# Optimization experiments

Hardware: AMD Instinct MI355X
Metric: run time of the kernel (lower is better)

Reference implementation:

```python
import jax, jax.numpy as jnp
import numpy as np

N, D, K = 32768, 512, 8192
TOPK = 3
BETA = 0.25  # commitment_cost
EPS = 1e-12  # F.normalize eps


def setup_inputs() -> dict:
    key = jax.random.key(0)
    k1, k2 = jax.random.split(key)
    x = jax.random.normal(k1, (N, D), dtype=jnp.float32)
    # nn.Embedding weight init: uniform(-1/num_embeddings, 1/num_embeddings)
    embeddings = jax.random.uniform(k2, (K, D), dtype=jnp.float32,
                                    minval=-1.0 / K, maxval=1.0 / K)
    return {"x": x, "embeddings": embeddings}


def _l2_normalize(v, axis):
    n = jnp.sqrt(jnp.sum(v * v, axis=axis, keepdims=True))
    return v / jnp.maximum(n, EPS)


def reference(x, embeddings):
    # --- get_code_indices ---
    xn = _l2_normalize(x, axis=1)              # [N, D]
    wn = _l2_normalize(embeddings, axis=1)     # [K, D]
    # squared euclidean distance between normalized vectors
    distances = (jnp.sum(xn * xn, axis=1, keepdims=True)
                 + jnp.sum(wn * wn, axis=1)
                 - 2.0 * jnp.einsum('nd,kd->nk', xn, wn))   # [N, K]
    neg_top, top_indices = jax.lax.top_k(-distances, TOPK)   # smallest distances
    top_values = -neg_top                                    # [N, TOPK]
    inv = 1.0 / top_values
    weights = inv / jnp.sum(inv, axis=1, keepdims=True)      # [N, TOPK]
    # --- quantize: gather UN-normalized codebook rows, weighted sum ---
    topk_quantized = embeddings[top_indices]                 # [N, TOPK, D]
    quantized = jnp.sum(topk_quantized * weights[..., None], axis=1)  # [N, D]
    # --- training losses + straight-through estimator ---
    q_latent_loss = jnp.mean((quantized - jax.lax.stop_gradient(x)) ** 2)
    e_latent_loss = jnp.mean((x - jax.lax.stop_gradient(quantized)) ** 2)
    loss = q_latent_loss + BETA * e_latent_loss
    quantized_st = x + jax.lax.stop_gradient(quantized - x)
    return quantized_st, loss, top_indices
```

## Files before the change

kernel.cpp:

```cpp
#include <hip/hip_runtime.h>
#include <cstdint>
#include <cstddef>

#define N_ROWS  32768
#define DIMS    512
#define K_CODES 8192

typedef short    bf16x8 __attribute__((ext_vector_type(8)));
typedef float    f32x4  __attribute__((ext_vector_type(4)));

__device__ __forceinline__ unsigned short cvt_bf16_rne(float f) {
  union { float f; unsigned u; } c; c.f = f;
  unsigned r = c.u + 0x7FFFu + ((c.u >> 16) & 1u);
  return (unsigned short)(r >> 16);
}


__device__ __forceinline__ float np_pairwise_sumsq_512(const float* buf, int l) {
  int blk = l >> 4, jv = (l >> 2) & 3, ln = l & 3;
  int cb = blk * 128 + jv * 4 + ln;
  float v = buf[cb];
  float r = __fmul_rn(v, v);
  #pragma unroll
  for (int i = 1; i < 8; ++i) {
    float t = buf[cb + 16 * i];
    r = __fadd_rn(r, __fmul_rn(t, t));
  }
  r = __fadd_rn(r, __shfl_xor(r, 4, 64));
  r = __fadd_rn(r, __shfl_xor(r, 8, 64));
  r = __fadd_rn(r, __shfl_xor(r, 1, 64));
  r = __fadd_rn(r, __shfl_xor(r, 2, 64));
  r = __fadd_rn(r, __shfl_xor(r, 16, 64));
  r = __fadd_rn(r, __shfl_xor(r, 32, 64));
  return r;
}

__global__ __launch_bounds__(256) void prep_x_kernel(
    const float* __restrict__ x, float* __restrict__ xninv) {
  int row = blockIdx.x * 4 + (threadIdx.x >> 6);
  int l = threadIdx.x & 63;
  const float* xr = x + (size_t)row * DIMS + l * 8;
  float4 a = *(const float4*)xr;
  float4 b = *(const float4*)(xr + 4);
  float s = a.x*a.x + a.y*a.y + a.z*a.z + a.w*a.w
          + b.x*b.x + b.y*b.y + b.z*b.z + b.w*b.w;
  #pragma unroll
  for (int off = 1; off < 64; off <<= 1) s += __shfl_xor(s, off, 64);
  float den = fmaxf(sqrtf(s), 1e-12f);
  if (l == 0) xninv[row] = 1.0f / den;
}

__global__ __launch_bounds__(256) void prep_w_np_kernel(
    const float* __restrict__ emb, float* __restrict__ den_w,
    float* __restrict__ wnorm2, unsigned short* __restrict__ wnh) {
  __shared__ float buf[4][512];
  int w = threadIdx.x >> 6, l = threadIdx.x & 63;
  int row = blockIdx.x * 4 + w;
  const float* wr = emb + (size_t)row * DIMS + l * 8;
  float4 a = *(const float4*)wr;
  float4 b = *(const float4*)(wr + 4);
  *(float4*)&buf[w][l * 8]     = a;
  *(float4*)&buf[w][l * 8 + 4] = b;
  __syncthreads();
  float S = np_pairwise_sumsq_512(buf[w], l);
  float den = fmaxf(__fsqrt_rn(S), 1e-12f);
  float nv[8];
  nv[0] = __fdiv_rn(a.x, den); nv[1] = __fdiv_rn(a.y, den);
  nv[2] = __fdiv_rn(a.z, den); nv[3] = __fdiv_rn(a.w, den);
  nv[4] = __fdiv_rn(b.x, den); nv[5] = __fdiv_rn(b.y, den);
  nv[6] = __fdiv_rn(b.z, den); nv[7] = __fdiv_rn(b.w, den);
  __syncthreads();
  *(float4*)&buf[w][l * 8]     = float4{nv[0], nv[1], nv[2], nv[3]};
  *(float4*)&buf[w][l * 8 + 4] = float4{nv[4], nv[5], nv[6], nv[7]};
  {
    unsigned hv[4];
    #pragma unroll
    for (int j = 0; j < 4; ++j) {
      unsigned lo = cvt_bf16_rne(nv[2*j]);
      unsigned hi = cvt_bf16_rne(nv[2*j + 1]);
      hv[j] = lo | (hi << 16);
    }
    *(uint4*)(wnh + (size_t)row * DIMS + l * 8) =
        uint4{hv[0], hv[1], hv[2], hv[3]};
  }
  __syncthreads();
  float S2 = np_pairwise_sumsq_512(buf[w], l);
  if (l == 0) { wnorm2[row] = S2; den_w[row] = den; }
}

#define MT_ROWS 128
#define MT_TILES 32
#define NSPLIT 4
#define SPLIT_COLS 2048
#define NROWGRP (N_ROWS / MT_ROWS)
#define BSTR_B 272
#define DSTR   33
#define QSTRIDE 32

__global__
__attribute__((amdgpu_flat_work_group_size(256, 256), amdgpu_waves_per_eu(2, 2)))
void mfma_topk_kernel(
    const float* __restrict__ x, const unsigned short* __restrict__ wnh,
    const float* __restrict__ xninv, unsigned* __restrict__ candk,
    unsigned* __restrict__ qctr) {
  __shared__ unsigned short Bs[64 * (BSTR_B / 2)];
  unsigned* dump = (unsigned*)Bs;
  __shared__ int s_rg, s_sp;

  const int tid = threadIdx.x;
  const int lane = tid & 63;
  const int wv = tid >> 6;
  const int l15 = lane & 15;
  const int lq = lane >> 4;

  if (tid == 0) {
    unsigned xcc;
    asm("s_getreg_b32 %0, hwreg(HW_REG_XCC_ID)" : "=s"(xcc));
    const int mysplit = (int)(xcc & 3);
    int rg = -1, sp = 0;
    #pragma unroll 1
    for (int i = 0; i < NSPLIT; ++i) {
      int s = (mysplit + i) & (NSPLIT - 1);
      unsigned r = atomicAdd(&qctr[s * QSTRIDE], 1u);
      if (r < (unsigned)NROWGRP) { rg = (int)r; sp = s; break; }
    }
    s_rg = rg; s_sp = sp;
  }
  __syncthreads();
  const int rowgrp = s_rg;
  const int split = s_sp;
  if (rowgrp < 0) return;
  const int row0 = rowgrp * MT_ROWS;
  const int col0 = split * SPLIT_COLS;

  const int scol = tid >> 2;
  const int spart = tid & 3;

  bf16x8 afrag[2][16];
  #pragma unroll
  for (int rs = 0; rs < 2; ++rs) {
    int row = row0 + wv * 32 + rs * 16 + l15;
    float sc = xninv[row];
    const float* xp = x + (size_t)row * DIMS + lq * 8;
    #pragma unroll
    for (int ks = 0; ks < 16; ++ks) {
      float4 a = *(const float4*)(xp + ks * 32);
      float4 b = *(const float4*)(xp + ks * 32 + 4);
      bf16x8 f;
      f[0] = (short)cvt_bf16_rne(a.x * sc); f[1] = (short)cvt_bf16_rne(a.y * sc);
      f[2] = (short)cvt_bf16_rne(a.z * sc); f[3] = (short)cvt_bf16_rne(a.w * sc);
      f[4] = (short)cvt_bf16_rne(b.x * sc); f[5] = (short)cvt_bf16_rne(b.y * sc);
      f[6] = (short)cvt_bf16_rne(b.z * sc); f[7] = (short)cvt_bf16_rne(b.w * sc);
      afrag[rs][ks] = f;
    }
  }

  unsigned m[8];
  #pragma unroll
  for (int j = 0; j < 8; ++j) m[j] = 0u;

  uint4 s0, s1, s2, s3;
  {
    const char* p = (const char*)wnh
        + ((size_t)(col0 + scol) * DIMS) * 2 + spart * 64;
    s0 = *(const uint4*)(p);
    s1 = *(const uint4*)(p + 16);
    s2 = *(const uint4*)(p + 32);
    s3 = *(const uint4*)(p + 48);
  }

  for (int t = 0; t < MT_TILES; ++t) {
    f32x4 acc[2][4];
    #pragma unroll
    for (int rs = 0; rs < 2; ++rs)
      #pragma unroll
      for (int cs = 0; cs < 4; ++cs)
        acc[rs][cs] = f32x4{0.f, 0.f, 0.f, 0.f};

    #pragma unroll
    for (int c = 0; c < 4; ++c) {
      __syncthreads();
      char* dst = (char*)Bs + scol * BSTR_B + spart * 64;
      *(uint4*)(dst)      = s0;
      *(uint4*)(dst + 16) = s1;
      *(uint4*)(dst + 32) = s2;
      *(uint4*)(dst + 48) = s3;
      int nt = t + ((c + 1) >> 2);
      int nc = (c + 1) & 3;
      if (nt < MT_TILES) {
        const char* p = (const char*)wnh
            + ((size_t)(col0 + nt * 64 + scol) * DIMS) * 2
            + nc * 256 + spart * 64;
        s0 = *(const uint4*)(p);
        s1 = *(const uint4*)(p + 16);
        s2 = *(const uint4*)(p + 32);
        s3 = *(const uint4*)(p + 48);
      }
      __syncthreads();
      #pragma unroll
      for (int kk = 0; kk < 4; ++kk) {
        const int ks = c * 4 + kk;
        bf16x8 bfr[4];
        #pragma unroll
        for (int cs = 0; cs < 4; ++cs)
          bfr[cs] = *(const bf16x8*)((const char*)Bs
                      + (cs * 16 + l15) * BSTR_B + kk * 64 + lq * 16);
        #pragma unroll
        for (int rs = 0; rs < 2; ++rs)
          #pragma unroll
          for (int cs = 0; cs < 4; ++cs)
            acc[rs][cs] = __builtin_amdgcn_mfma_f32_16x16x32_bf16(
                afrag[rs][ks], bfr[cs], acc[rs][cs], 0, 0, 0);
      }
    }
    __syncthreads();

    #pragma unroll
    for (int rs = 0; rs < 2; ++rs)
      #pragma unroll
      for (int rg2 = 0; rg2 < 4; ++rg2) {
        unsigned kkey[4];
        #pragma unroll
        for (int cs = 0; cs < 4; ++cs) {
          float v = acc[rs][cs][rg2];
          union { float f; unsigned u; } cu;
          cu.f = fmaf(v, 0.5f, 2.5f);
          kkey[cs] = ((cu.u << 9) & 0xFFFFF000u)
                   | (unsigned)(t * 64 + cs * 16 + l15);
        }
        unsigned h1 = max(kkey[0], kkey[1]), lo1 = min(kkey[0], kkey[1]);
        unsigned h2 = max(kkey[2], kkey[3]), lo2 = min(kkey[2], kkey[3]);
        unsigned m1 = max(h1, h2);
        unsigned m2 = max(min(h1, h2), max(lo1, lo2));
        int rowl = wv * 32 + rs * 16 + lq * 4 + rg2;
        dump[rowl * DSTR + l15 * 2 + 0] = m1;
        dump[rowl * DSTR + l15 * 2 + 1] = m2;
      }
    __syncthreads();

    {
      int srow = tid & 127;
      int qb = (tid >> 7) * 16;
      #pragma unroll
      for (int q = 0; q < 16; ++q) {
        unsigned cv = dump[srow * DSTR + qb + q];
        #pragma unroll
        for (int j = 0; j < 8; ++j) {
          unsigned hi = max(m[j], cv), lo = min(m[j], cv);
          m[j] = hi; cv = lo;
        }
      }
    }
  }

  __syncthreads();
  if (tid >= 128) {
    #pragma unroll
    for (int j = 0; j < 8; ++j) dump[(tid & 127) * DSTR + 16 + j] = m[j];
  }
  __syncthreads();
  if (tid < 128) {
    #pragma unroll
    for (int j = 0; j < 8; ++j) {
      unsigned cv = dump[tid * DSTR + 16 + j];
      #pragma unroll
      for (int jj = 0; jj < 8; ++jj) {
        unsigned hi = max(m[jj], cv), lo = min(m[jj], cv);
        m[jj] = hi; cv = lo;
      }
    }
    unsigned* o = candk + (size_t)(row0 + tid) * 32 + split * 8;
    #pragma unroll
    for (int j = 0; j < 8; ++j) o[j] = m[j];
  }
}

#define WSTR 516

__global__ __launch_bounds__(256, 3) void refine_mfma_kernel(
    const float* __restrict__ x, const float* __restrict__ emb,
    const float* __restrict__ den_w, const float* __restrict__ wnorm2,
    const unsigned* __restrict__ candk,
    float* __restrict__ out, double* __restrict__ lossparts) {
  __shared__ float xbuf[4][512];
  __shared__ float wbuf4[4][4 * WSTR];
  int w = threadIdx.x >> 6, l = threadIdx.x & 63;
  int row = blockIdx.x * 4 + w;

  const float* xr = x + (size_t)row * DIMS + l * 8;
  float4 x0 = *(const float4*)xr;
  float4 x1 = *(const float4*)(xr + 4);
  *(float4*)&xbuf[w][l * 8]     = x0;
  *(float4*)&xbuf[w][l * 8 + 4] = x1;
  __syncthreads();
  float Sx = np_pairwise_sumsq_512(xbuf[w], l);
  float denx = fmaxf(__fsqrt_rn(Sx), 1e-12f);
  float xn[8];
  xn[0] = __fdiv_rn(x0.x, denx); xn[1] = __fdiv_rn(x0.y, denx);
  xn[2] = __fdiv_rn(x0.z, denx); xn[3] = __fdiv_rn(x0.w, denx);
  xn[4] = __fdiv_rn(x1.x, denx); xn[5] = __fdiv_rn(x1.y, denx);
  xn[6] = __fdiv_rn(x1.z, denx); xn[7] = __fdiv_rn(x1.w, denx);
  __syncthreads();
  *(float4*)&xbuf[w][l * 8]     = float4{xn[0], xn[1], xn[2], xn[3]};
  *(float4*)&xbuf[w][l * 8 + 4] = float4{xn[4], xn[5], xn[6], xn[7]};
  __syncthreads();
  float xn2 = np_pairwise_sumsq_512(xbuf[w], l);

  unsigned val = 0u; int col = 0x7fffffff;
  if (l < 32) {
    unsigned key = candk[(size_t)row * 32 + l];
    val = key >> 12;
    col = (l >> 3) * SPLIT_COLS + (int)(key & 0xFFFu);
  }

  int k8[8];
  #pragma unroll
  for (int it = 0; it < 8; ++it) {
    unsigned mv = val; int mk = col;
    #pragma unroll
    for (int off = 1; off < 64; off <<= 1) {
      unsigned ov = (unsigned)__shfl_xor((int)mv, off, 64);
      int ok = __shfl_xor(mk, off, 64);
      bool take = (ov > mv) || (ov == mv && ok < mk);
      mv = take ? ov : mv; mk = take ? ok : mk;
    }
    k8[it] = mk;
    if (col == mk) val = 0u;
  }

  float4 ga[4], gb[4];
  #pragma unroll
  for (int c = 0; c < 4; ++c) {
    const float* wr = emb + (size_t)k8[c] * DIMS + l * 8;
    ga[c] = *(const float4*)wr;
    gb[c] = *(const float4*)(wr + 4);
  }

  float d8[8];
  #pragma unroll
  for (int g = 0; g < 2; ++g) {
    #pragma unroll
    for (int c = 0; c < 4; ++c) {
      float dk = den_w[k8[g * 4 + c]];
      *(float4*)&wbuf4[w][c * WSTR + l * 8] =
          float4{__fdiv_rn(ga[c].x, dk), __fdiv_rn(ga[c].y, dk),
                 __fdiv_rn(ga[c].z, dk), __fdiv_rn(ga[c].w, dk)};
      *(float4*)&wbuf4[w][c * WSTR + l * 8 + 4] =
          float4{__fdiv_rn(gb[c].x, dk), __fdiv_rn(gb[c].y, dk),
                 __fdiv_rn(gb[c].z, dk), __fdiv_rn(gb[c].w, dk)};
    }
    if (g == 0) {
      #pragma unroll
      for (int c = 0; c < 4; ++c) {
        const float* wr = emb + (size_t)k8[4 + c] * DIMS + l * 8;
        ga[c] = *(const float4*)wr;
        gb[c] = *(const float4*)(wr + 4);
      }
    }
    __syncthreads();

    {
      int j = l & 3;
      const float* xp = xbuf[w];
      const float* wp = &wbuf4[w][j * WSTR];
      float t = 0.f;
      #pragma unroll 8
      for (int d = 0; d < 512; ++d) t = fmaf(xp[d], wp[d], t);
      #pragma unroll
      for (int c = 0; c < 4; ++c) {
        float dot = __shfl(t, c, 64);
        float s = __fadd_rn(xn2, wnorm2[k8[g * 4 + c]]);
        d8[g * 4 + c] = __fadd_rn(s, -(2.0f * dot));
      }
    }
    __syncthreads();
  }

  {
    float bd[3]; int bk[3];
    #pragma unroll
    for (int s = 0; s < 3; ++s) {
      float mv = INFINITY; int mk = 0x7fffffff;
      #pragma unroll
      for (int it = 0; it < 8; ++it) {
        bool take = (d8[it] < mv) || (d8[it] == mv && k8[it] < mk);
        mv = take ? d8[it] : mv; mk = take ? k8[it] : mk;
      }
      bd[s] = mv; bk[s] = mk;
      #pragma unroll
      for (int it = 0; it < 8; ++it)
        if (k8[it] == mk) d8[it] = INFINITY;
    }

    double i0 = 1.0 / (double)bd[0], i1 = 1.0 / (double)bd[1],
           i2 = 1.0 / (double)bd[2];
    double tot = (i0 + i1) + i2;
    double w0q = i0 / tot, w1q = i1 / tot, w2q = i2 / tot;

    if (l == 0) {
      float* oi = out + (size_t)N_ROWS * DIMS + 1 + (size_t)row * 3;
      oi[0] = (float)bk[0]; oi[1] = (float)bk[1]; oi[2] = (float)bk[2];
    }

    const float* e0 = emb + (size_t)bk[0] * DIMS + l * 8;
    const float* e1 = emb + (size_t)bk[1] * DIMS + l * 8;
    const float* e2 = emb + (size_t)bk[2] * DIMS + l * 8;
    float4 ea0 = *(const float4*)e0, eb0 = *(const float4*)(e0 + 4);
    float4 ea1 = *(const float4*)e1, eb1 = *(const float4*)(e1 + 4);
    float4 ea2 = *(const float4*)e2, eb2 = *(const float4*)(e2 + 4);
    double xs[8];
    xs[0] = x0.x; xs[1] = x0.y; xs[2] = x0.z; xs[3] = x0.w;
    xs[4] = x1.x; xs[5] = x1.y; xs[6] = x1.z; xs[7] = x1.w;
    double q[8];
    q[0] = w0q*(double)ea0.x + w1q*(double)ea1.x + w2q*(double)ea2.x;
    q[1] = w0q*(double)ea0.y + w1q*(double)ea1.y + w2q*(double)ea2.y;
    q[2] = w0q*(double)ea0.z + w1q*(double)ea1.z + w2q*(double)ea2.z;
    q[3] = w0q*(double)ea0.w + w1q*(double)ea1.w + w2q*(double)ea2.w;
    q[4] = w0q*(double)eb0.x + w1q*(double)eb1.x + w2q*(double)eb2.x;
    q[5] = w0q*(double)eb0.y + w1q*(double)eb1.y + w2q*(double)eb2.y;
    q[6] = w0q*(double)eb0.z + w1q*(double)eb1.z + w2q*(double)eb2.z;
    q[7] = w0q*(double)eb0.w + w1q*(double)eb1.w + w2q*(double)eb2.w;

    double lp = 0.0;
    float o[8];
    #pragma unroll
    for (int jj = 0; jj < 8; ++jj) {
      double diff = q[jj] - xs[jj];
      o[jj] = (float)(xs[jj] + diff);
      lp += diff * diff;
    }
    float* orow = out + (size_t)row * DIMS + l * 8;
    *(float4*)orow       = float4{o[0], o[1], o[2], o[3]};
    *(float4*)(orow + 4) = float4{o[4], o[5], o[6], o[7]};

    #pragma unroll
    for (int off = 1; off < 64; off <<= 1) lp += __shfl_xor(lp, off, 64);
    if (l == 0) lossparts[row] = lp;
  }
}

__global__ __launch_bounds__(256) void loss_finalize_kernel(
    const double* __restrict__ lossparts, float* __restrict__ out) {
  __shared__ double sred[4];
  int tid = threadIdx.x;
  double s = 0.0;
  for (int i = tid; i < N_ROWS; i += 256) s += lossparts[i];
  #pragma unroll
  for (int off = 1; off < 64; off <<= 1) s += __shfl_xor(s, off, 64);
  if ((tid & 63) == 0) sred[tid >> 6] = s;
  __syncthreads();
  if (tid == 0) {
    double m = (((sred[0] + sred[1]) + sred[2]) + sred[3]) / 16777216.0;
    out[(size_t)N_ROWS * DIMS] = (float)(m + 0.25 * m);
  }
}

extern "C" void kernel_launch(void* const* d_in, const int* in_sizes, int n_in,
                              void* d_out, int out_size, void* d_ws, size_t ws_size,
                              hipStream_t stream) {
  (void)in_sizes; (void)n_in; (void)out_size; (void)ws_size;
  const float* x   = (const float*)d_in[0];
  const float* emb = (const float*)d_in[1];
  float* out = (float*)d_out;
  char* ws = (char*)d_ws;

  float*          wnorm2    = (float*)(ws);
  float*          den_w     = (float*)(ws + 32768);
  float*          xninv     = (float*)(ws + 65536);
  unsigned short* wnh       = (unsigned short*)(ws + 196608);
  unsigned*       candk     = (unsigned*)(ws + 8585216);
  double*         lossparts = (double*)(ws + 12779520);
  unsigned*       qctr      = (unsigned*)(ws + 13041664);

  prep_w_np_kernel<<<K_CODES / 4, 256, 0, stream>>>(emb, den_w, wnorm2, wnh);
  prep_x_kernel<<<N_ROWS / 4, 256, 0, stream>>>(x, xninv);
  hipMemsetAsync(qctr, 0, 512, stream);
  mfma_topk_kernel<<<NROWGRP * NSPLIT, 256, 0, stream>>>(
      x, wnh, xninv, candk, qctr);
  refine_mfma_kernel<<<N_ROWS / 4, 256, 0, stream>>>(
      x, emb, den_w, wnorm2, candk, out, lossparts);
  loss_finalize_kernel<<<1, 256, 0, stream>>>(lossparts, out);
}
```

Before: 746.4 us.

## Use 512-thread blocks with one 16-row strip per wave in top-k GEMM

Block size of the MFMA top-k kernel doubles from 256 to 512 threads. Each of the 8 waves now owns 16 rows instead of 32, which halves the A-fragment and accumulator registers per wave, and the occupancy hint rises from 2 to 4 waves per EU. B-tile staging is split across twice as many threads, and the final merge now folds three partial top-8 lists into the first group. Each wave does half as many MFMAs per B-fragment load from LDS, so LDS read traffic per MFMA doubles and the serial final merge gets longer.

```diff
diff --git a/kernel.cpp b/kernel.cpp
--- a/kernel.cpp
+++ b/kernel.cpp
@@ -98,7 +98,7 @@
 #define QSTRIDE 32
 
 __global__
-__attribute__((amdgpu_flat_work_group_size(256, 256), amdgpu_waves_per_eu(2, 2)))
+__attribute__((amdgpu_flat_work_group_size(512, 512), amdgpu_waves_per_eu(4, 4)))
 void mfma_topk_kernel(
     const float* __restrict__ x, const unsigned short* __restrict__ wnh,
     const float* __restrict__ xninv, unsigned* __restrict__ candk,
@@ -133,13 +133,12 @@
   const int row0 = rowgrp * MT_ROWS;
   const int col0 = split * SPLIT_COLS;
 
-  const int scol = tid >> 2;
-  const int spart = tid & 3;
-
-  bf16x8 afrag[2][16];
-  #pragma unroll
-  for (int rs = 0; rs < 2; ++rs) {
-    int row = row0 + wv * 32 + rs * 16 + l15;
+  const int scol = tid >> 3;
+  const int spart = tid & 7;
+
+  bf16x8 afrag[16];
+  {
+    int row = row0 + wv * 16 + l15;
     float sc = xninv[row];
     const float* xp = x + (size_t)row * DIMS + lq * 8;
     #pragma unroll
@@ -151,7 +150,7 @@
       f[2] = (short)cvt_bf16_rne(a.z * sc); f[3] = (short)cvt_bf16_rne(a.w * sc);
       f[4] = (short)cvt_bf16_rne(b.x * sc); f[5] = (short)cvt_bf16_rne(b.y * sc);
       f[6] = (short)cvt_bf16_rne(b.z * sc); f[7] = (short)cvt_bf16_rne(b.w * sc);
-      afrag[rs][ks] = f;
+      afrag[ks] = f;
     }
   }
 
@@ -159,42 +158,34 @@
   #pragma unroll
   for (int j = 0; j < 8; ++j) m[j] = 0u;
 
-  uint4 s0, s1, s2, s3;
+  uint4 s0, s1;
   {
     const char* p = (const char*)wnh
-        + ((size_t)(col0 + scol) * DIMS) * 2 + spart * 64;
+        + ((size_t)(col0 + scol) * DIMS) * 2 + spart * 32;
     s0 = *(const uint4*)(p);
     s1 = *(const uint4*)(p + 16);
-    s2 = *(const uint4*)(p + 32);
-    s3 = *(const uint4*)(p + 48);
   }
 
   for (int t = 0; t < MT_TILES; ++t) {
-    f32x4 acc[2][4];
-    #pragma unroll
-    for (int rs = 0; rs < 2; ++rs)
-      #pragma unroll
-      for (int cs = 0; cs < 4; ++cs)
-        acc[rs][cs] = f32x4{0.f, 0.f, 0.f, 0.f};
+    f32x4 acc[4];
+    #pragma unroll
+    for (int cs = 0; cs < 4; ++cs)
+      acc[cs] = f32x4{0.f, 0.f, 0.f, 0.f};
 
     #pragma unroll
     for (int c = 0; c < 4; ++c) {
       __syncthreads();
-      char* dst = (char*)Bs + scol * BSTR_B + spart * 64;
+      char* dst = (char*)Bs + scol * BSTR_B + spart * 32;
       *(uint4*)(dst)      = s0;
       *(uint4*)(dst + 16) = s1;
-      *(uint4*)(dst + 32) = s2;
-      *(uint4*)(dst + 48) = s3;
       int nt = t + ((c + 1) >> 2);
       int nc = (c + 1) & 3;
       if (nt < MT_TILES) {
         const char* p = (const char*)wnh
             + ((size_t)(col0 + nt * 64 + scol) * DIMS) * 2
-            + nc * 256 + spart * 64;
+            + nc * 256 + spart * 32;
         s0 = *(const uint4*)(p);
         s1 = *(const uint4*)(p + 16);
-        s2 = *(const uint4*)(p + 32);
-        s3 = *(const uint4*)(p + 48);
       }
       __syncthreads();
       #pragma unroll
@@ -206,43 +197,39 @@
           bfr[cs] = *(const bf16x8*)((const char*)Bs
                       + (cs * 16 + l15) * BSTR_B + kk * 64 + lq * 16);
         #pragma unroll
-        for (int rs = 0; rs < 2; ++rs)
-          #pragma unroll
-          for (int cs = 0; cs < 4; ++cs)
-            acc[rs][cs] = __builtin_amdgcn_mfma_f32_16x16x32_bf16(
-                afrag[rs][ks], bfr[cs], acc[rs][cs], 0, 0, 0);
+        for (int cs = 0; cs < 4; ++cs)
+          acc[cs] = __builtin_amdgcn_mfma_f32_16x16x32_bf16(
+              afrag[ks], bfr[cs], acc[cs], 0, 0, 0);
       }
     }
     __syncthreads();
 
     #pragma unroll
-    for (int rs = 0; rs < 2; ++rs)
-      #pragma unroll
-      for (int rg2 = 0; rg2 < 4; ++rg2) {
-        unsigned kkey[4];
-        #pragma unroll
-        for (int cs = 0; cs < 4; ++cs) {
-          float v = acc[rs][cs][rg2];
-          union { float f; unsigned u; } cu;
-          cu.f = fmaf(v, 0.5f, 2.5f);
-          kkey[cs] = ((cu.u << 9) & 0xFFFFF000u)
-                   | (unsigned)(t * 64 + cs * 16 + l15);
-        }
-        unsigned h1 = max(kkey[0], kkey[1]), lo1 = min(kkey[0], kkey[1]);
-        unsigned h2 = max(kkey[2], kkey[3]), lo2 = min(kkey[2], kkey[3]);
-        unsigned m1 = max(h1, h2);
-        unsigned m2 = max(min(h1, h2), max(lo1, lo2));
-        int rowl = wv * 32 + rs * 16 + lq * 4 + rg2;
-        dump[rowl * DSTR + l15 * 2 + 0] = m1;
-        dump[rowl * DSTR + l15 * 2 + 1] = m2;
-      }
+    for (int rg2 = 0; rg2 < 4; ++rg2) {
+      unsigned kkey[4];
+      #pragma unroll
+      for (int cs = 0; cs < 4; ++cs) {
+        float v = acc[cs][rg2];
+        union { float f; unsigned u; } cu;
+        cu.f = fmaf(v, 0.5f, 2.5f);
+        kkey[cs] = ((cu.u << 9) & 0xFFFFF000u)
+                 | (unsigned)(t * 64 + cs * 16 + l15);
+      }
+      unsigned h1 = max(kkey[0], kkey[1]), lo1 = min(kkey[0], kkey[1]);
+      unsigned h2 = max(kkey[2], kkey[3]), lo2 = min(kkey[2], kkey[3]);
+      unsigned m1 = max(h1, h2);
+      unsigned m2 = max(min(h1, h2), max(lo1, lo2));
+      int rowl = wv * 16 + lq * 4 + rg2;
+      dump[rowl * DSTR + l15 * 2 + 0] = m1;
+      dump[rowl * DSTR + l15 * 2 + 1] = m2;
+    }
     __syncthreads();
 
     {
       int srow = tid & 127;
-      int qb = (tid >> 7) * 16;
-      #pragma unroll
-      for (int q = 0; q < 16; ++q) {
+      int qb = (tid >> 7) * 8;
+      #pragma unroll
+      for (int q = 0; q < 8; ++q) {
         unsigned cv = dump[srow * DSTR + qb + q];
         #pragma unroll
         for (int j = 0; j < 8; ++j) {
@@ -254,24 +241,28 @@
   }
 
   __syncthreads();
-  if (tid >= 128) {
-    #pragma unroll
-    for (int j = 0; j < 8; ++j) dump[(tid & 127) * DSTR + 16 + j] = m[j];
-  }
-  __syncthreads();
-  if (tid < 128) {
-    #pragma unroll
-    for (int j = 0; j < 8; ++j) {
-      unsigned cv = dump[tid * DSTR + 16 + j];
-      #pragma unroll
-      for (int jj = 0; jj < 8; ++jj) {
-        unsigned hi = max(m[jj], cv), lo = min(m[jj], cv);
-        m[jj] = hi; cv = lo;
-      }
-    }
-    unsigned* o = candk + (size_t)(row0 + tid) * 32 + split * 8;
-    #pragma unroll
-    for (int j = 0; j < 8; ++j) o[j] = m[j];
+  {
+    int g = tid >> 7;
+    int srow = tid & 127;
+    if (g > 0) {
+      #pragma unroll
+      for (int j = 0; j < 8; ++j) dump[srow * DSTR + (g - 1) * 8 + j] = m[j];
+    }
+    __syncthreads();
+    if (g == 0) {
+      #pragma unroll 1
+      for (int e = 0; e < 24; ++e) {
+        unsigned cv = dump[srow * DSTR + e];
+        #pragma unroll
+        for (int jj = 0; jj < 8; ++jj) {
+          unsigned hi = max(m[jj], cv), lo = min(m[jj], cv);
+          m[jj] = hi; cv = lo;
+        }
+      }
+      unsigned* o = candk + (size_t)(row0 + srow) * 32 + split * 8;
+      #pragma unroll
+      for (int j = 0; j < 8; ++j) o[j] = m[j];
+    }
   }
 }
 
@@ -475,7 +466,7 @@
   prep_w_np_kernel<<<K_CODES / 4, 256, 0, stream>>>(emb, den_w, wnorm2, wnh);
   prep_x_kernel<<<N_ROWS / 4, 256, 0, stream>>>(x, xninv);
   hipMemsetAsync(qctr, 0, 512, stream);
-  mfma_topk_kernel<<<NROWGRP * NSPLIT, 256, 0, stream>>>(
+  mfma_topk_kernel<<<NROWGRP * NSPLIT, 512, 0, stream>>>(
       x, wnh, xninv, candk, qctr);
   refine_mfma_kernel<<<N_ROWS / 4, 256, 0, stream>>>(
       x, emb, den_w, wnorm2, candk, out, lossparts);
```

Result: slower. 777.1 us (+4.1%).
